# Optimization experiments

Measured on AMD Instinct MI355X. Metric: run time of the kernel, lower is better.

The kernel has to match this reference:

```python
import jax, jax.numpy as jnp
import numpy as np
import math

B, S, D = 8, 1024, 1024
H, R = 16, 8
HD = D // H
SCALING = 16.0 / R  # alpha / rank = 2.0
DFF = 4 * D
DC = D // 2
NC = 3


def setup_inputs() -> dict:
    key = jax.random.key(0)
    ks = jax.random.split(key, 32)
    n = lambda i, shape, s=0.02: jax.random.normal(ks[i], shape, dtype=jnp.float32) * s
    inp = {
        'hidden_states': jax.random.normal(ks[0], (B, S, D), dtype=jnp.float32),
        # LoRA-adapted projections: base weight W [out,in], lora_A [r,in], lora_B [out,r]
        'Wq': n(1, (D, D)), 'Aq': n(2, (R, D), 0.1), 'Bq': n(3, (D, R), 0.02),
        'Wk': n(4, (D, D)), 'Ak': n(5, (R, D), 0.1), 'Bk': n(6, (D, R), 0.02),
        'Wv': n(7, (D, D)), 'Av': n(8, (R, D), 0.1), 'Bv': n(9, (D, R), 0.02),
        'Wo': n(10, (D, D)), 'Ao': n(11, (R, D), 0.1), 'Bo': n(12, (D, R), 0.02),
        'ln1_g': jnp.ones((D,), jnp.float32), 'ln1_b': jnp.zeros((D,), jnp.float32),
        'ln2_g': jnp.ones((D,), jnp.float32), 'ln2_b': jnp.zeros((D,), jnp.float32),
        'W1': n(13, (DFF, D)), 'b1': jnp.zeros((DFF,), jnp.float32),
        'W2': n(14, (D, DFF)), 'b2': jnp.zeros((D,), jnp.float32),
        'Wc1': n(15, (DC, D)), 'bc1': jnp.zeros((DC,), jnp.float32),
        'Wc2': n(16, (NC, DC)), 'bc2': jnp.zeros((NC,), jnp.float32),
    }
    return inp


def _lora_linear(x, W, A, Bm):
    # F.linear(x, W) + scaling * F.linear(F.linear(x, A), B)
    return x @ W.T + SCALING * ((x @ A.T) @ Bm.T)


def _layer_norm(x, g, b, eps=1e-5):
    mu = jnp.mean(x, axis=-1, keepdims=True)
    var = jnp.var(x, axis=-1, keepdims=True)
    return (x - mu) * jax.lax.rsqrt(var + eps) * g + b


def reference(hidden_states, Wq, Aq, Bq, Wk, Ak, Bk, Wv, Av, Bv, Wo, Ao, Bo,
              ln1_g, ln1_b, ln2_g, ln2_b, W1, b1, W2, b2, Wc1, bc1, Wc2, bc2):
    residual = hidden_states
    h = _layer_norm(hidden_states, ln1_g, ln1_b)
    # attention
    q = _lora_linear(h, Wq, Aq, Bq).reshape(B, S, H, HD).transpose(0, 2, 1, 3)
    k = _lora_linear(h, Wk, Ak, Bk).reshape(B, S, H, HD).transpose(0, 2, 1, 3)
    v = _lora_linear(h, Wv, Av, Bv).reshape(B, S, H, HD).transpose(0, 2, 1, 3)
    scores = jnp.einsum('bhqd,bhkd->bhqk', q, k) / math.sqrt(HD)
    probs = jax.nn.softmax(scores, axis=-1)
    ctx = jnp.einsum('bhqk,bhkd->bhqd', probs, v)
    ctx = ctx.transpose(0, 2, 1, 3).reshape(B, S, D)
    attn_out = _lora_linear(ctx, Wo, Ao, Bo)
    h = residual + attn_out
    residual = h
    hn = _layer_norm(h, ln2_g, ln2_b)
    ffn = jax.nn.gelu(hn @ W1.T + b1, approximate=False) @ W2.T + b2
    h = residual + ffn
    pooled = h[:, 0]  # [B, D]
    logits = jax.nn.gelu(pooled @ Wc1.T + bc1, approximate=False) @ Wc2.T + bc2
    return logits
```

## Files before the change

### kernel.cpp

```cpp
#include <hip/hip_runtime.h>
#include <hip/hip_bf16.h>


__device__ __forceinline__ float blo(unsigned int u) {
  union { unsigned int i; float f; } v; v.i = u << 16; return v.f;
}
__device__ __forceinline__ float bhi(unsigned int u) {
  union { unsigned int i; float f; } v; v.i = u & 0xffff0000u; return v.f;
}
__device__ __forceinline__ unsigned short f2bf(float f) {
  union { float f; unsigned int i; } v; v.f = f;
  unsigned int u = v.i;
  u += 0x7FFFu + ((u >> 16) & 1u);
  return (unsigned short)(u >> 16);
}
__device__ __forceinline__ float gelu_exact(float x) {
  return 0.5f * x * (1.0f + erff(x * 0.70710678118654752440f));
}
__device__ __forceinline__ float wave_sum(float v) {
#pragma unroll
  for (int o = 1; o < 64; o <<= 1) v += __shfl_xor(v, o);
  return v;
}

__global__ __launch_bounds__(256) void ln_fused(
    const float* __restrict__ x, const float* __restrict__ g,
    const float* __restrict__ b, unsigned short* __restrict__ hbf,
    float* __restrict__ x0) {
  int blk = blockIdx.x;
  int f32out = (blk >= 8192);
  const float* xr = f32out ? (x + (size_t)(blk - 8192) * 1048576)
                           : (x + (size_t)blk * 1024);
  int t = threadIdx.x, w = t >> 6, l = t & 63;
  float4 v = ((const float4*)xr)[t];
  float s  = v.x + v.y + v.z + v.w;
  float sq = v.x * v.x + v.y * v.y + v.z * v.z + v.w * v.w;
#pragma unroll
  for (int o = 32; o; o >>= 1) { s += __shfl_down(s, o); sq += __shfl_down(sq, o); }
  __shared__ float rs_[4], rq_[4], stat[2];
  if (l == 0) { rs_[w] = s; rq_[w] = sq; }
  __syncthreads();
  if (t == 0) {
    float S = rs_[0] + rs_[1] + rs_[2] + rs_[3];
    float Q = rq_[0] + rq_[1] + rq_[2] + rq_[3];
    float mu = S * (1.0f / 1024.0f);
    float var = Q * (1.0f / 1024.0f) - mu * mu;
    stat[0] = mu; stat[1] = rsqrtf(var + 1e-5f);
  }
  __syncthreads();
  float mu = stat[0], rstd = stat[1];
  float4 gg = ((const float4*)g)[t];
  float4 bb = ((const float4*)b)[t];
  float o0 = (v.x - mu) * rstd * gg.x + bb.x;
  float o1 = (v.y - mu) * rstd * gg.y + bb.y;
  float o2 = (v.z - mu) * rstd * gg.z + bb.z;
  float o3 = (v.w - mu) * rstd * gg.w + bb.w;
  if (f32out) {
    float* op = x0 + (size_t)(blk - 8192) * 1024 + t * 4;
    op[0] = o0; op[1] = o1; op[2] = o2; op[3] = o3;
  } else {
    unsigned short* op = hbf + (size_t)blk * 1024 + t * 4;
    op[0] = f2bf(o0); op[1] = f2bf(o1); op[2] = f2bf(o2); op[3] = f2bf(o3);
  }
}

template <int CPW>
__global__ __launch_bounds__(256) void skinny_gemm(
    const float* __restrict__ X, long xrs, long xhs,
    const float* __restrict__ W, const float* __restrict__ bias,
    const float* __restrict__ Amat, const float* __restrict__ Bmat,
    const float* __restrict__ resid, long rstride,
    float* __restrict__ Y, int N, int K, int do_gelu) {
  __shared__ float sX[8][1024];
  __shared__ float sT[8][8][4];
  __shared__ float T[8][8];
  int t = threadIdx.x, w = t >> 6, l = t & 63;
  int bcol = blockIdx.x * (4 * CPW);
  int col0 = bcol + w * CPW;
  int head = bcol >> 6;
  const float* Xb = X + (size_t)head * xhs;
  float acc[CPW][8];
#pragma unroll
  for (int c = 0; c < CPW; ++c)
#pragma unroll
    for (int m = 0; m < 8; ++m) acc[c][m] = 0.f;
  for (int kc = 0; kc < K; kc += 1024) {
    for (int i = t; i < 2048; i += 256) {
      int m = i >> 8, p = i & 255;
      ((float4*)sX[m])[p] = *(const float4*)(Xb + (size_t)m * xrs + kc + p * 4);
    }
    __syncthreads();
    if (Amat && kc == 0) {
      int m = t >> 5, r = (t >> 2) & 7, q = t & 3;
      float s = 0.f;
      const float* ar = Amat + r * 1024 + q * 256;
      const float* xr = &sX[m][q * 256];
      for (int j = 0; j < 256; j += 4)
        s += xr[j] * ar[j] + xr[j+1] * ar[j+1] + xr[j+2] * ar[j+2] + xr[j+3] * ar[j+3];
      sT[m][r][q] = s;
      __syncthreads();
      if (t < 64) {
        int mm = t >> 3, rr = t & 7;
        T[mm][rr] = sT[mm][rr][0] + sT[mm][rr][1] + sT[mm][rr][2] + sT[mm][rr][3];
      }
      __syncthreads();
    }
#pragma unroll
    for (int i = 0; i < 4; ++i) {
      int k = i * 256 + l * 4;
      float4 xv[8];
#pragma unroll
      for (int m = 0; m < 8; ++m) xv[m] = *(const float4*)&sX[m][k];
#pragma unroll
      for (int c = 0; c < CPW; ++c) {
        float4 wv = *(const float4*)(W + (size_t)(col0 + c) * K + kc + k);
#pragma unroll
        for (int m = 0; m < 8; ++m)
          acc[c][m] += wv.x * xv[m].x + wv.y * xv[m].y + wv.z * xv[m].z + wv.w * xv[m].w;
      }
    }
    __syncthreads();
  }
#pragma unroll
  for (int c = 0; c < CPW; ++c)
#pragma unroll
    for (int m = 0; m < 8; ++m) {
      float v = acc[c][m];
#pragma unroll
      for (int o = 32; o; o >>= 1) v += __shfl_down(v, o);
      acc[c][m] = v;
    }
  if (l == 0) {
#pragma unroll
    for (int c = 0; c < CPW; ++c) {
      int col = col0 + c;
      float bv = bias ? bias[col] : 0.f;
      float lb[8];
      if (Amat) {
#pragma unroll
        for (int r = 0; r < 8; ++r) lb[r] = Bmat[col * 8 + r];
      }
#pragma unroll
      for (int m = 0; m < 8; ++m) {
        float v = acc[c][m] + bv;
        if (Amat) {
#pragma unroll
          for (int r = 0; r < 8; ++r) v += 2.0f * lb[r] * T[m][r];
        }
        if (do_gelu) v = gelu_exact(v);
        if (resid) v += resid[(size_t)m * rstride + col];
        Y[(size_t)m * N + col] = v;
      }
    }
  }
}

__global__ __launch_bounds__(256) void pullback_kernel(
    const float* __restrict__ q0, const float* __restrict__ Wk,
    const float* __restrict__ Ak, const float* __restrict__ Bk,
    float* __restrict__ qh) {
  int head = blockIdx.x >> 2, cchunk = blockIdx.x & 3;
  int t = threadIdx.x;
  int c = cchunk * 256 + t;
  __shared__ float sq[8][64];
  __shared__ float sT[8][8][4];
  __shared__ float T[8][8];
  if (t < 512) { int b = t >> 6, d = t & 63; sq[b][d] = q0[b * 1024 + head * 64 + d]; }
  __syncthreads();
  {
    int b = t >> 5, r = (t >> 2) & 7, q = t & 3;
    float s = 0.f;
#pragma unroll
    for (int j = 0; j < 16; ++j) {
      int d = q * 16 + j;
      s += sq[b][d] * Bk[(head * 64 + d) * 8 + r];
    }
    sT[b][r][q] = s;
  }
  __syncthreads();
  if (t < 64) {
    int b = t >> 3, r = t & 7;
    T[b][r] = sT[b][r][0] + sT[b][r][1] + sT[b][r][2] + sT[b][r][3];
  }
  __syncthreads();
  float acc[8] = {0.f, 0.f, 0.f, 0.f, 0.f, 0.f, 0.f, 0.f};
#pragma unroll 4
  for (int d = 0; d < 64; ++d) {
    float wv = Wk[(size_t)(head * 64 + d) * 1024 + c];
#pragma unroll
    for (int b = 0; b < 8; ++b) acc[b] += sq[b][d] * wv;
  }
  float av[8];
#pragma unroll
  for (int r = 0; r < 8; ++r) av[r] = Ak[r * 1024 + c];
#pragma unroll
  for (int b = 0; b < 8; ++b) {
    float v = acc[b];
#pragma unroll
    for (int r = 0; r < 8; ++r) v += 2.0f * T[b][r] * av[r];
    qh[(size_t)(head * 8 + b) * 1024 + c] = v;
  }
}

__global__ __launch_bounds__(512) void attn_flash(
    const float* __restrict__ qh, const unsigned short* __restrict__ hbf,
    float* __restrict__ opart, float* __restrict__ ml) {
  int b = blockIdx.x & 7, kc = blockIdx.x >> 3;
  int t = threadIdx.x, wid = t >> 6, l = t & 63;
  __shared__ float S[32][16];
  __shared__ float smax[16];
  __shared__ float pS[32][16];
  const unsigned short* hb = hbf + (size_t)b * 1048576 + (size_t)kc * 32768;
  float qv[2][16];
#pragma unroll
  for (int hi = 0; hi < 2; ++hi) {
    const float4* qp = (const float4*)(qh + (size_t)((hi * 8 + wid) * 8 + b) * 1024 + l * 16);
#pragma unroll
    for (int i = 0; i < 4; ++i) {
      float4 q4 = qp[i];
      qv[hi][i * 4 + 0] = q4.x; qv[hi][i * 4 + 1] = q4.y;
      qv[hi][i * 4 + 2] = q4.z; qv[hi][i * 4 + 3] = q4.w;
    }
  }
  for (int k = 0; k < 32; ++k) {
    const uint4* hp = (const uint4*)(hb + (size_t)k * 1024 + l * 16);
    uint4 u0 = hp[0], u1 = hp[1];
    float hv[16];
    hv[0]=blo(u0.x); hv[1]=bhi(u0.x); hv[2]=blo(u0.y); hv[3]=bhi(u0.y);
    hv[4]=blo(u0.z); hv[5]=bhi(u0.z); hv[6]=blo(u0.w); hv[7]=bhi(u0.w);
    hv[8]=blo(u1.x); hv[9]=bhi(u1.x); hv[10]=blo(u1.y); hv[11]=bhi(u1.y);
    hv[12]=blo(u1.z); hv[13]=bhi(u1.z); hv[14]=blo(u1.w); hv[15]=bhi(u1.w);
    float s0 = 0.f, s1 = 0.f;
#pragma unroll
    for (int j = 0; j < 16; ++j) { s0 += qv[0][j] * hv[j]; s1 += qv[1][j] * hv[j]; }
    s0 = wave_sum(s0); s1 = wave_sum(s1);
    if (l == 0) {
      S[k][wid]     = s0 * 0.125f;
      S[k][wid + 8] = s1 * 0.125f;
    }
  }
  __syncthreads();
  if (t < 16) {
    float m = -1e30f;
    for (int k = 0; k < 32; ++k) m = fmaxf(m, S[k][t]);
    float ls = 0.f;
    for (int k = 0; k < 32; ++k) ls += expf(S[k][t] - m);
    smax[t] = m;
    ml[((size_t)(b * 32 + kc) * 16 + t) * 2]     = m;
    ml[((size_t)(b * 32 + kc) * 16 + t) * 2 + 1] = ls;
  }
  __syncthreads();
  { int k = t >> 4, h = t & 15;
    pS[k][h] = expf(S[k][h] - smax[h]); }
  __syncthreads();
  int c0 = t * 2;
  float a0[16], a1[16];
#pragma unroll
  for (int h = 0; h < 16; ++h) { a0[h] = 0.f; a1[h] = 0.f; }
  for (int k = 0; k < 32; ++k) {
    unsigned int u = *(const unsigned int*)(hb + (size_t)k * 1024 + c0);
    float h0 = blo(u), h1 = bhi(u);
    float4 p0 = *(const float4*)&pS[k][0];
    float4 p1 = *(const float4*)&pS[k][4];
    float4 p2 = *(const float4*)&pS[k][8];
    float4 p3 = *(const float4*)&pS[k][12];
    float pk[16] = {p0.x, p0.y, p0.z, p0.w, p1.x, p1.y, p1.z, p1.w,
                    p2.x, p2.y, p2.z, p2.w, p3.x, p3.y, p3.z, p3.w};
#pragma unroll
    for (int h = 0; h < 16; ++h) { a0[h] += pk[h] * h0; a1[h] += pk[h] * h1; }
  }
  float* ob = opart + ((size_t)(b * 32 + kc) * 16) * 1024 + c0;
#pragma unroll
  for (int h = 0; h < 16; ++h) {
    float2 o2; o2.x = a0[h]; o2.y = a1[h];
    *(float2*)(ob + (size_t)h * 1024) = o2;
  }
}

__global__ __launch_bounds__(256) void combine_kernel(
    const float* __restrict__ opart, const float* __restrict__ ml,
    float* __restrict__ pv) {
  int blk = blockIdx.x;
  int hh = blk >> 3, b = blk & 7;
  int t = threadIdx.x;
  __shared__ float am[32], al[32], e[32], Linv;
  if (t < 32) {
    am[t] = ml[((size_t)(b * 32 + t) * 16 + hh) * 2];
    al[t] = ml[((size_t)(b * 32 + t) * 16 + hh) * 2 + 1];
  }
  __syncthreads();
  if (t == 0) {
    float M = -1e30f;
    for (int c = 0; c < 32; ++c) M = fmaxf(M, am[c]);
    float L = 0.f;
    for (int c = 0; c < 32; ++c) {
      float ee = expf(am[c] - M);
      e[c] = ee;
      L += al[c] * ee;
    }
    Linv = 1.f / L;
  }
  __syncthreads();
  int c0 = t * 4;
  float4 a = (float4){0.f, 0.f, 0.f, 0.f};
#pragma unroll 8
  for (int kc = 0; kc < 32; ++kc) {
    float4 v = *(const float4*)(opart + ((size_t)(b * 32 + kc) * 16 + hh) * 1024 + c0);
    float ee = e[kc];
    a.x += ee * v.x; a.y += ee * v.y; a.z += ee * v.z; a.w += ee * v.w;
  }
  float inv = Linv;
  a.x *= inv; a.y *= inv; a.z *= inv; a.w *= inv;
  *(float4*)(pv + (size_t)(hh * 8 + b) * 1024 + c0) = a;
}

__global__ __launch_bounds__(256) void ln2_ffn1(
    const float* __restrict__ h2, const float* __restrict__ g,
    const float* __restrict__ bb, const float* __restrict__ W1,
    const float* __restrict__ b1, float* __restrict__ mid,
    const float* __restrict__ bc2, float* __restrict__ out) {
  __shared__ float sX[8][1024];
  int t = threadIdx.x, w = t >> 6, l = t & 63;
  if (blockIdx.x == 0 && t < 24) out[t] = bc2[t % 3];
  for (int i = t; i < 2048; i += 256)
    ((float4*)sX)[i] = ((const float4*)h2)[i];
  __syncthreads();
#pragma unroll
  for (int rr = 0; rr < 2; ++rr) {
    int r = w + rr * 4;
    float4 xv[4];
#pragma unroll
    for (int i = 0; i < 4; ++i) xv[i] = *(const float4*)&sX[r][i * 256 + l * 4];
    float s = 0.f, sq = 0.f;
#pragma unroll
    for (int i = 0; i < 4; ++i) {
      s  += xv[i].x + xv[i].y + xv[i].z + xv[i].w;
      sq += xv[i].x * xv[i].x + xv[i].y * xv[i].y + xv[i].z * xv[i].z + xv[i].w * xv[i].w;
    }
    s = wave_sum(s); sq = wave_sum(sq);
    float mu = s * (1.f / 1024.f);
    float rstd = rsqrtf(sq * (1.f / 1024.f) - mu * mu + 1e-5f);
#pragma unroll
    for (int i = 0; i < 4; ++i) {
      float4 g4 = ((const float4*)g)[i * 64 + l];
      float4 b4 = ((const float4*)bb)[i * 64 + l];
      float4 o;
      o.x = (xv[i].x - mu) * rstd * g4.x + b4.x;
      o.y = (xv[i].y - mu) * rstd * g4.y + b4.y;
      o.z = (xv[i].z - mu) * rstd * g4.z + b4.z;
      o.w = (xv[i].w - mu) * rstd * g4.w + b4.w;
      *(float4*)&sX[r][i * 256 + l * 4] = o;
    }
  }
  __syncthreads();
  int col0 = blockIdx.x * 16 + w * 4;
  float acc[4][8];
#pragma unroll
  for (int c = 0; c < 4; ++c)
#pragma unroll
    for (int m = 0; m < 8; ++m) acc[c][m] = 0.f;
#pragma unroll
  for (int i = 0; i < 4; ++i) {
    int k = i * 256 + l * 4;
    float4 xv[8];
#pragma unroll
    for (int m = 0; m < 8; ++m) xv[m] = *(const float4*)&sX[m][k];
#pragma unroll
    for (int c = 0; c < 4; ++c) {
      float4 wv = *(const float4*)(W1 + (size_t)(col0 + c) * 1024 + k);
#pragma unroll
      for (int m = 0; m < 8; ++m)
        acc[c][m] += wv.x * xv[m].x + wv.y * xv[m].y + wv.z * xv[m].z + wv.w * xv[m].w;
    }
  }
#pragma unroll
  for (int c = 0; c < 4; ++c)
#pragma unroll
    for (int m = 0; m < 8; ++m) acc[c][m] = wave_sum(acc[c][m]);
  if (l == 0) {
#pragma unroll
    for (int c = 0; c < 4; ++c) {
      int col = col0 + c;
      float bv = b1[col];
#pragma unroll
      for (int m = 0; m < 8; ++m)
        mid[(size_t)m * 4096 + col] = gelu_exact(acc[c][m] + bv);
    }
  }
}

__global__ __launch_bounds__(256) void cls_logits(
    const float* __restrict__ pooled, const float* __restrict__ Wc1,
    const float* __restrict__ bc1, const float* __restrict__ Wc2,
    float* __restrict__ out) {
  __shared__ float sX[8][1024];
  __shared__ float plog[4][8][3];
  int t = threadIdx.x, w = t >> 6, l = t & 63;
  for (int i = t; i < 2048; i += 256)
    ((float4*)sX)[i] = ((const float4*)pooled)[i];
  __syncthreads();
  float preg[8][3];
#pragma unroll
  for (int m = 0; m < 8; ++m)
#pragma unroll
    for (int n = 0; n < 3; ++n) preg[m][n] = 0.f;
  for (int ci = 0; ci < 4; ++ci) {
    int col = blockIdx.x * 16 + w * 4 + ci;
    float acc[8] = {0.f, 0.f, 0.f, 0.f, 0.f, 0.f, 0.f, 0.f};
#pragma unroll
    for (int i = 0; i < 4; ++i) {
      int k = i * 256 + l * 4;
      float4 wv = *(const float4*)(Wc1 + (size_t)col * 1024 + k);
#pragma unroll
      for (int m = 0; m < 8; ++m) {
        float4 xv = *(const float4*)&sX[m][k];
        acc[m] += wv.x * xv.x + wv.y * xv.y + wv.z * xv.z + wv.w * xv.w;
      }
    }
#pragma unroll
    for (int m = 0; m < 8; ++m) acc[m] = wave_sum(acc[m]);
    if (l == 0) {
#pragma unroll
      for (int m = 0; m < 8; ++m) {
        float v = gelu_exact(acc[m] + bc1[col]);
#pragma unroll
        for (int n = 0; n < 3; ++n) preg[m][n] += v * Wc2[n * 512 + col];
      }
    }
  }
  if (l == 0) {
#pragma unroll
    for (int m = 0; m < 8; ++m)
#pragma unroll
      for (int n = 0; n < 3; ++n) plog[w][m][n] = preg[m][n];
  }
  __syncthreads();
  if (t < 24) {
    int m = t / 3, n = t % 3;
    float v = plog[0][m][n] + plog[1][m][n] + plog[2][m][n] + plog[3][m][n];
    atomicAdd(&out[t], v);
  }
}

extern "C" void kernel_launch(void* const* d_in, const int* in_sizes, int n_in,
                              void* d_out, int out_size, void* d_ws, size_t ws_size,
                              hipStream_t stream) {
  const float* x    = (const float*)d_in[0];
  const float* Wq   = (const float*)d_in[1];
  const float* Aq   = (const float*)d_in[2];
  const float* Bq   = (const float*)d_in[3];
  const float* Wk   = (const float*)d_in[4];
  const float* Ak   = (const float*)d_in[5];
  const float* Bk   = (const float*)d_in[6];
  const float* Wv   = (const float*)d_in[7];
  const float* Av   = (const float*)d_in[8];
  const float* Bv   = (const float*)d_in[9];
  const float* Wo   = (const float*)d_in[10];
  const float* Ao   = (const float*)d_in[11];
  const float* Bo   = (const float*)d_in[12];
  const float* ln1g = (const float*)d_in[13];
  const float* ln1b = (const float*)d_in[14];
  const float* ln2g = (const float*)d_in[15];
  const float* ln2b = (const float*)d_in[16];
  const float* W1   = (const float*)d_in[17];
  const float* b1   = (const float*)d_in[18];
  const float* W2   = (const float*)d_in[19];
  const float* b2   = (const float*)d_in[20];
  const float* Wc1  = (const float*)d_in[21];
  const float* bc1  = (const float*)d_in[22];
  const float* Wc2  = (const float*)d_in[23];
  const float* bc2  = (const float*)d_in[24];

  char* ws = (char*)d_ws;
  size_t off = 0;
  auto alloc = [&](size_t bytes) {
    void* p = ws + off;
    off += (bytes + 255) & ~(size_t)255;
    return p;
  };
  unsigned short* h_bf = (unsigned short*)alloc((size_t)8192 * 1024 * 2);
  float* qh      = (float*)alloc((size_t)128 * 1024 * 4);
  float* opart   = (float*)alloc((size_t)256 * 16 * 1024 * 4);
  float* ml      = (float*)alloc((size_t)8 * 32 * 16 * 2 * 4);
  float* pvb     = (float*)alloc((size_t)128 * 1024 * 4);
  float* x0   = (float*)alloc(8 * 1024 * 4);
  float* q0   = (float*)alloc(8 * 1024 * 4);
  float* ctx0 = (float*)alloc(8 * 1024 * 4);
  float* h2   = (float*)alloc(8 * 1024 * 4);
  float* mid  = (float*)alloc(8 * 4096 * 4);
  float* pooled = (float*)alloc(8 * 1024 * 4);

  ln_fused<<<8200, 256, 0, stream>>>(x, ln1g, ln1b, h_bf, x0);
  skinny_gemm<1><<<256, 256, 0, stream>>>(x0, 1024, 0, Wq, nullptr, Aq, Bq,
                                          nullptr, 0, q0, 1024, 1024, 0);
  pullback_kernel<<<64, 256, 0, stream>>>(q0, Wk, Ak, Bk, qh);
  attn_flash<<<256, 512, 0, stream>>>(qh, h_bf, opart, ml);
  combine_kernel<<<128, 256, 0, stream>>>(opart, ml, pvb);
  skinny_gemm<1><<<256, 256, 0, stream>>>(pvb, 1024, 8192, Wv, nullptr, Av, Bv,
                                          nullptr, 0, ctx0, 1024, 1024, 0);
  skinny_gemm<1><<<256, 256, 0, stream>>>(ctx0, 1024, 0, Wo, nullptr, Ao, Bo,
                                          x, 1048576, h2, 1024, 1024, 0);
  ln2_ffn1<<<256, 256, 0, stream>>>(h2, ln2g, ln2b, W1, b1, mid, bc2,
                                    (float*)d_out);
  skinny_gemm<1><<<256, 256, 0, stream>>>(mid, 4096, 0, W2, b2, nullptr, nullptr,
                                          h2, 1024, pooled, 1024, 4096, 0);
  cls_logits<<<32, 256, 0, stream>>>(pooled, Wc1, bc1, Wc2, (float*)d_out);
}
```

Measured before the change: 158.2 us.

## Replace split-softmax combine kernel with atomic accumulation and deferred normalization

The attention kernel now skips the per-chunk max subtraction, exponentiates scores directly, and atomically adds unnormalized partial PV outputs and row sums into global buffers. The first layernorm kernel zeroes those buffers, and the V-projection GEMM divides by the accumulated sum. This removes the combine kernel launch and the large partial-output write and read. In exchange it drops max-stabilization, which risks overflow for large scores, adds contention on float atomics, and makes the summation order nondeterministic.

```diff
diff --git a/kernel.cpp b/kernel.cpp
--- a/kernel.cpp
+++ b/kernel.cpp
@@ -26,7 +26,7 @@
 __global__ __launch_bounds__(256) void ln_fused(
     const float* __restrict__ x, const float* __restrict__ g,
     const float* __restrict__ b, unsigned short* __restrict__ hbf,
-    float* __restrict__ x0) {
+    float* __restrict__ x0, float* __restrict__ pvb, float* __restrict__ Lbuf) {
   int blk = blockIdx.x;
   int f32out = (blk >= 8192);
   const float* xr = f32out ? (x + (size_t)(blk - 8192) * 1048576)
@@ -58,6 +58,10 @@
   if (f32out) {
     float* op = x0 + (size_t)(blk - 8192) * 1024 + t * 4;
     op[0] = o0; op[1] = o1; op[2] = o2; op[3] = o3;
+    int zt = (blk - 8192) * 256 + t;
+    float4 z4 = {0.f, 0.f, 0.f, 0.f};
+    for (int i = zt; i < 32768; i += 2048) ((float4*)pvb)[i] = z4;
+    if (zt < 128) Lbuf[zt] = 0.f;
   } else {
     unsigned short* op = hbf + (size_t)blk * 1024 + t * 4;
     op[0] = f2bf(o0); op[1] = f2bf(o1); op[2] = f2bf(o2); op[3] = f2bf(o3);
@@ -70,6 +74,7 @@
     const float* __restrict__ W, const float* __restrict__ bias,
     const float* __restrict__ Amat, const float* __restrict__ Bmat,
     const float* __restrict__ resid, long rstride,
+    const float* __restrict__ Ldiv,
     float* __restrict__ Y, int N, int K, int do_gelu) {
   __shared__ float sX[8][1024];
   __shared__ float sT[8][8][4];
@@ -147,6 +152,7 @@
 #pragma unroll
           for (int r = 0; r < 8; ++r) v += 2.0f * lb[r] * T[m][r];
         }
+        if (Ldiv) v /= Ldiv[head * 8 + m];
         if (do_gelu) v = gelu_exact(v);
         if (resid) v += resid[(size_t)m * rstride + col];
         Y[(size_t)m * N + col] = v;
@@ -202,13 +208,12 @@
   }
 }
 
-__global__ __launch_bounds__(512) void attn_flash(
+__global__ __launch_bounds__(512) void attn_atomic(
     const float* __restrict__ qh, const unsigned short* __restrict__ hbf,
-    float* __restrict__ opart, float* __restrict__ ml) {
+    float* __restrict__ pvb, float* __restrict__ Lbuf) {
   int b = blockIdx.x & 7, kc = blockIdx.x >> 3;
   int t = threadIdx.x, wid = t >> 6, l = t & 63;
   __shared__ float S[32][16];
-  __shared__ float smax[16];
   __shared__ float pS[32][16];
   const unsigned short* hb = hbf + (size_t)b * 1048576 + (size_t)kc * 32768;
   float qv[2][16];
@@ -240,19 +245,14 @@
     }
   }
   __syncthreads();
+  { int k = t >> 4, h = t & 15;
+    pS[k][h] = expf(S[k][h]); }
+  __syncthreads();
   if (t < 16) {
-    float m = -1e30f;
-    for (int k = 0; k < 32; ++k) m = fmaxf(m, S[k][t]);
     float ls = 0.f;
-    for (int k = 0; k < 32; ++k) ls += expf(S[k][t] - m);
-    smax[t] = m;
-    ml[((size_t)(b * 32 + kc) * 16 + t) * 2]     = m;
-    ml[((size_t)(b * 32 + kc) * 16 + t) * 2 + 1] = ls;
-  }
-  __syncthreads();
-  { int k = t >> 4, h = t & 15;
-    pS[k][h] = expf(S[k][h] - smax[h]); }
-  __syncthreads();
+    for (int k = 0; k < 32; ++k) ls += pS[k][t];
+    atomicAdd(&Lbuf[t * 8 + b], ls);
+  }
   int c0 = t * 2;
   float a0[16], a1[16];
 #pragma unroll
@@ -269,49 +269,12 @@
 #pragma unroll
     for (int h = 0; h < 16; ++h) { a0[h] += pk[h] * h0; a1[h] += pk[h] * h1; }
   }
-  float* ob = opart + ((size_t)(b * 32 + kc) * 16) * 1024 + c0;
 #pragma unroll
   for (int h = 0; h < 16; ++h) {
-    float2 o2; o2.x = a0[h]; o2.y = a1[h];
-    *(float2*)(ob + (size_t)h * 1024) = o2;
-  }
-}
-
-__global__ __launch_bounds__(256) void combine_kernel(
-    const float* __restrict__ opart, const float* __restrict__ ml,
-    float* __restrict__ pv) {
-  int blk = blockIdx.x;
-  int hh = blk >> 3, b = blk & 7;
-  int t = threadIdx.x;
-  __shared__ float am[32], al[32], e[32], Linv;
-  if (t < 32) {
-    am[t] = ml[((size_t)(b * 32 + t) * 16 + hh) * 2];
-    al[t] = ml[((size_t)(b * 32 + t) * 16 + hh) * 2 + 1];
-  }
-  __syncthreads();
-  if (t == 0) {
-    float M = -1e30f;
-    for (int c = 0; c < 32; ++c) M = fmaxf(M, am[c]);
-    float L = 0.f;
-    for (int c = 0; c < 32; ++c) {
-      float ee = expf(am[c] - M);
-      e[c] = ee;
-      L += al[c] * ee;
-    }
-    Linv = 1.f / L;
-  }
-  __syncthreads();
-  int c0 = t * 4;
-  float4 a = (float4){0.f, 0.f, 0.f, 0.f};
-#pragma unroll 8
-  for (int kc = 0; kc < 32; ++kc) {
-    float4 v = *(const float4*)(opart + ((size_t)(b * 32 + kc) * 16 + hh) * 1024 + c0);
-    float ee = e[kc];
-    a.x += ee * v.x; a.y += ee * v.y; a.z += ee * v.z; a.w += ee * v.w;
-  }
-  float inv = Linv;
-  a.x *= inv; a.y *= inv; a.z *= inv; a.w *= inv;
-  *(float4*)(pv + (size_t)(hh * 8 + b) * 1024 + c0) = a;
+    float* dst = pvb + (size_t)(h * 8 + b) * 1024 + c0;
+    atomicAdd(dst, a0[h]);
+    atomicAdd(dst + 1, a1[h]);
+  }
 }
 
 __global__ __launch_bounds__(256) void ln2_ffn1(
@@ -480,9 +443,8 @@
   };
   unsigned short* h_bf = (unsigned short*)alloc((size_t)8192 * 1024 * 2);
   float* qh      = (float*)alloc((size_t)128 * 1024 * 4);
-  float* opart   = (float*)alloc((size_t)256 * 16 * 1024 * 4);
-  float* ml      = (float*)alloc((size_t)8 * 32 * 16 * 2 * 4);
   float* pvb     = (float*)alloc((size_t)128 * 1024 * 4);
+  float* Lbuf    = (float*)alloc(128 * 4);
   float* x0   = (float*)alloc(8 * 1024 * 4);
   float* q0   = (float*)alloc(8 * 1024 * 4);
   float* ctx0 = (float*)alloc(8 * 1024 * 4);
@@ -490,19 +452,18 @@
   float* mid  = (float*)alloc(8 * 4096 * 4);
   float* pooled = (float*)alloc(8 * 1024 * 4);
 
-  ln_fused<<<8200, 256, 0, stream>>>(x, ln1g, ln1b, h_bf, x0);
+  ln_fused<<<8200, 256, 0, stream>>>(x, ln1g, ln1b, h_bf, x0, pvb, Lbuf);
   skinny_gemm<1><<<256, 256, 0, stream>>>(x0, 1024, 0, Wq, nullptr, Aq, Bq,
-                                          nullptr, 0, q0, 1024, 1024, 0);
+                                          nullptr, 0, nullptr, q0, 1024, 1024, 0);
   pullback_kernel<<<64, 256, 0, stream>>>(q0, Wk, Ak, Bk, qh);
-  attn_flash<<<256, 512, 0, stream>>>(qh, h_bf, opart, ml);
-  combine_kernel<<<128, 256, 0, stream>>>(opart, ml, pvb);
+  attn_atomic<<<256, 512, 0, stream>>>(qh, h_bf, pvb, Lbuf);
   skinny_gemm<1><<<256, 256, 0, stream>>>(pvb, 1024, 8192, Wv, nullptr, Av, Bv,
-                                          nullptr, 0, ctx0, 1024, 1024, 0);
+                                          nullptr, 0, Lbuf, ctx0, 1024, 1024, 0);
   skinny_gemm<1><<<256, 256, 0, stream>>>(ctx0, 1024, 0, Wo, nullptr, Ao, Bo,
-                                          x, 1048576, h2, 1024, 1024, 0);
+                                          x, 1048576, nullptr, h2, 1024, 1024, 0);
   ln2_ffn1<<<256, 256, 0, stream>>>(h2, ln2g, ln2b, W1, b1, mid, bc2,
                                     (float*)d_out);
   skinny_gemm<1><<<256, 256, 0, stream>>>(mid, 4096, 0, W2, b2, nullptr, nullptr,
-                                          h2, 1024, pooled, 1024, 4096, 0);
+                                          h2, 1024, nullptr, pooled, 1024, 4096, 0);
   cls_logits<<<32, 256, 0, stream>>>(pooled, Wc1, bc1, Wc2, (float*)d_out);
 }
```

Result: slower. 189.1 us (+19.5%).
